# Kernel tuning notes

Measured on AMD Instinct MI355X. Metric: run time of the kernel, lower is better.

## Reference

```python
import jax, jax.numpy as jnp
import numpy as np


def _att(h, g, adj, a1, a2):
    # h: [B,N,D], g: [B,M,D], adj: [B,N,M] (int), a1/a2: [D,1]
    e1 = jnp.matmul(h, a1)                    # [B,N,1]
    e2 = jnp.matmul(g, a2).transpose(0, 2, 1)  # [B,1,M]
    e = jax.nn.leaky_relu(e1 + e2, negative_slope=0.2)  # [B,N,M]
    neg = jnp.asarray(-9.0e15, e.dtype)
    att = jnp.where(adj > 0, e, neg)
    att = jax.nn.softmax(att, axis=2)
    att = jnp.where(jnp.isnan(att), jnp.zeros_like(att), att)
    # degree renorm: adj[bs].sum(1).repeat(M,1).T == row degree broadcast over M
    deg = jnp.sum(adj, axis=2, keepdims=True).astype(e.dtype)  # [B,N,1]
    return jnp.matmul(att * deg, g)            # [B,N,D]


def setup_inputs() -> dict:
    key = jax.random.key(0)
    ks = jax.random.split(key, 13)
    B, N1, N2 = 64, 1024, 512
    F0, F1, D = 512, 384, 256
    return {
        "x0": jax.random.normal(ks[0], (B, N1, F0), jnp.float32),
        "x1": jax.random.normal(ks[1], (B, N2, F1), jnp.float32),
        "W0": jax.random.normal(ks[2], (F0, D), jnp.float32) * (1.414 / np.sqrt(F0)),
        "W1": jax.random.normal(ks[3], (F1, D), jnp.float32) * (1.414 / np.sqrt(F1)),
        "a1_0": jax.random.normal(ks[4], (D, 1), jnp.float32) * 0.1,
        "a2_0": jax.random.normal(ks[5], (D, 1), jnp.float32) * 0.1,
        "a1_1": jax.random.normal(ks[6], (D, 1), jnp.float32) * 0.1,
        "a2_1": jax.random.normal(ks[7], (D, 1), jnp.float32) * 0.1,
        "bias": jax.random.uniform(ks[8], (D,), jnp.float32, -1.0 / np.sqrt(D), 1.0 / np.sqrt(D)),
        "adj00": jax.random.randint(ks[9], (B, N1, N1), 0, 2, jnp.int32),
        "adj01": jax.random.randint(ks[10], (B, N1, N2), 0, 2, jnp.int32),
        "adj10": jax.random.randint(ks[11], (B, N2, N1), 0, 2, jnp.int32),
        "adj11": jax.random.randint(ks[12], (B, N2, N2), 0, 2, jnp.int32),
    }


def reference(x0, x1, W0, W1, a1_0, a2_0, a1_1, a2_1, bias,
              adj00, adj01, adj10, adj11):
    h0 = jnp.matmul(x0, W0)  # [B,N1,D]
    h1 = jnp.matmul(x1, W1)  # [B,N2,D]
    o00 = _att(h0, h0, adj00, a1_0, a2_0) + bias
    o01 = _att(h0, h1, adj01, a1_0, a2_0) + bias
    o10 = _att(h1, h0, adj10, a1_1, a2_1) + bias
    o11 = _att(h1, h1, adj11, a1_1, a2_1) + bias
    return (o00, o01, o10, o11)
```

## Files before the change

kernel.cpp:

```cpp
#include <hip/hip_runtime.h>

typedef __bf16 bf16x8 __attribute__((ext_vector_type(8)));
typedef float f32x4 __attribute__((ext_vector_type(4)));

static __device__ __forceinline__ ushort f2bf(float f) {
  uint u = __builtin_bit_cast(uint, f);
  u += 0x7fffu + ((u >> 16) & 1u);
  return (ushort)(u >> 16);
}
static __device__ __forceinline__ float bf2f(ushort h) {
  uint u = ((uint)h) << 16;
  return __builtin_bit_cast(float, u);
}

__global__ void detect9(const ushort* p0, const ushort* p1, const ushort* p2,
                        const ushort* p3, const ushort* p4, const ushort* p5,
                        const ushort* p6, const ushort* p7, const ushort* p8,
                        int* flags) {
  const ushort* ps[9] = {p0, p1, p2, p3, p4, p5, p6, p7, p8};
  const ushort* p = ps[blockIdx.x];
  int t = threadIdx.x;
  ushort u = p[2 * t];
  int e = (u >> 7) & 0xFF;
  int sane = (e >= 100 && e <= 150) ? 1 : 0;
  unsigned long long m = __ballot(sane);
  if (t == 0) flags[blockIdx.x] = (__popcll(m) >= 48) ? 0 : 1;
}

static __device__ __forceinline__ float ldf(const void* p, int is32, size_t i) {
  return is32 ? ((const float*)p)[i] : bf2f(((const ushort*)p)[i]);
}

__global__ void transw(const void* W, ushort* __restrict__ WT,
                       const int* __restrict__ flags, int fi, int F) {
  int is32 = flags[fi];
  int i = blockIdx.x * 256 + threadIdx.x;
  int k = i >> 8, d = i & 255;
  ushort v = is32 ? f2bf(((const float*)W)[i]) : ((const ushort*)W)[i];
  WT[(size_t)d * F + k] = v;
}

__global__ __launch_bounds__(256) void wa_k(const void* W, const void* a1, const void* a2,
                                            const void* a3, const int* __restrict__ flags,
                                            int fW, int f1, int f2, int f3,
                                            float* __restrict__ wa, int F) {
  __shared__ float al[3][256];
  int t = threadIdx.x;
  al[0][t] = ldf(a1, flags[f1], t);
  al[1][t] = ldf(a2, flags[f2], t);
  al[2][t] = ldf(a3, flags[f3], t);
  __syncthreads();
  int k = blockIdx.x * 256 + t;
  if (k < F) {
    int w32 = flags[fW];
    float s0 = 0.f, s1 = 0.f, s2 = 0.f;
    for (int d = 0; d < 256; d++) {
      float wv = ldf(W, w32, (size_t)k * 256 + d);
      s0 += wv * al[0][d]; s1 += wv * al[1][d]; s2 += wv * al[2][d];
    }
    wa[k] = s0; wa[F + k] = s1; wa[2 * F + k] = s2;
  }
}

__global__ __launch_bounds__(256) void evec_x(const void* __restrict__ x,
                                              const float* __restrict__ wa,
                                              const int* __restrict__ flags, int fi,
                                              float* __restrict__ o1, float* __restrict__ o2,
                                              float* __restrict__ o3, int F) {
  int x32 = flags[fi];
  int node = blockIdx.x * 4 + (threadIdx.x >> 6);
  int lane = threadIdx.x & 63;
  const float* wa1 = wa, *wa2 = wa + F, *wa3 = wa + 2 * F;
  float s1 = 0.f, s2 = 0.f, s3 = 0.f;
  size_t base = (size_t)node * F;
  for (int k = lane; k < F; k += 64) {
    float xv = ldf(x, x32, base + k);
    s1 += xv * wa1[k]; s2 += xv * wa2[k]; s3 += xv * wa3[k];
  }
  #pragma unroll
  for (int off = 1; off < 64; off <<= 1) {
    s1 += __shfl_xor(s1, off); s2 += __shfl_xor(s2, off); s3 += __shfl_xor(s3, off);
  }
  if (lane == 0) { o1[node] = s1; o2[node] = s2; o3[node] = s3; }
}

__global__ __launch_bounds__(256) void gemm_h(const void* __restrict__ x,
                                              const ushort* __restrict__ WT,
                                              ushort* __restrict__ hT,
                                              const int* __restrict__ flags, int fi,
                                              int N, int F) {
  int x32 = flags[fi];
  int ntiles = N >> 6;
  int b  = blockIdx.x / ntiles;
  int n0 = (blockIdx.x % ntiles) << 6;
  __shared__ ushort Al[64][72];
  __shared__ ushort Bl[256][72];
  int t = threadIdx.x, wave = t >> 6, lane = t & 63;
  f32x4 acc[4][4] = {};

  for (int k0 = 0; k0 < F; k0 += 64) {
    #pragma unroll
    for (int i = 0; i < 2; i++) {
      int r = (t >> 3) + i * 32, g = t & 7;
      if (!x32) {
        const ushort* xb = (const ushort*)x + (size_t)(b * N + n0 + r) * F + k0;
        ((uint4*)&Al[r][0])[g] = ((const uint4*)xb)[g];
      } else {
        const float* xf = (const float*)x + (size_t)(b * N + n0 + r) * F + k0;
        float4 fa = ((const float4*)xf)[2 * g];
        float4 fb = ((const float4*)xf)[2 * g + 1];
        union { ushort u[8]; uint4 q; } pk;
        pk.u[0] = f2bf(fa.x); pk.u[1] = f2bf(fa.y); pk.u[2] = f2bf(fa.z); pk.u[3] = f2bf(fa.w);
        pk.u[4] = f2bf(fb.x); pk.u[5] = f2bf(fb.y); pk.u[6] = f2bf(fb.z); pk.u[7] = f2bf(fb.w);
        ((uint4*)&Al[r][0])[g] = pk.q;
      }
    }
    #pragma unroll
    for (int i = 0; i < 8; i++) {
      int d = (t >> 3) + i * 32, g = t & 7;
      ((uint4*)&Bl[d][0])[g] = ((const uint4*)(WT + (size_t)d * F + k0))[g];
    }
    __syncthreads();
    #pragma unroll
    for (int kh = 0; kh < 2; kh++) {
      int kk = kh * 32 + ((lane >> 4) << 3);
      bf16x8 af[4], bfr[4];
      #pragma unroll
      for (int rf = 0; rf < 4; rf++) af[rf]  = *(const bf16x8*)&Al[rf * 16 + (lane & 15)][kk];
      #pragma unroll
      for (int cf = 0; cf < 4; cf++) bfr[cf] = *(const bf16x8*)&Bl[wave * 64 + cf * 16 + (lane & 15)][kk];
      #pragma unroll
      for (int rf = 0; rf < 4; rf++)
        #pragma unroll
        for (int cf = 0; cf < 4; cf++)
          acc[rf][cf] = __builtin_amdgcn_mfma_f32_16x16x32_bf16(af[rf], bfr[cf], acc[rf][cf], 0, 0, 0);
    }
    __syncthreads();
  }
  #pragma unroll
  for (int rf = 0; rf < 4; rf++) {
    int n = n0 + rf * 16 + ((lane >> 4) << 2);
    #pragma unroll
    for (int cf = 0; cf < 4; cf++) {
      int d = wave * 64 + cf * 16 + (lane & 15);
      ushort4 v;
      v.x = f2bf(acc[rf][cf][0]); v.y = f2bf(acc[rf][cf][1]);
      v.z = f2bf(acc[rf][cf][2]); v.w = f2bf(acc[rf][cf][3]);
      *(ushort4*)(hT + ((size_t)b * 256 + d) * N + n) = v;
    }
  }
}

__global__ __launch_bounds__(256) void att(const float* __restrict__ e1,
                                           const float* __restrict__ e2,
                                           const ushort* __restrict__ gT,
                                           const int* __restrict__ adj,
                                           const void* bias,
                                           const int* __restrict__ flags,
                                           void* __restrict__ outv, size_t ooff,
                                           int Nr, int M) {
  int b32 = flags[8];
  int o32 = flags[0] | flags[1] | flags[2] | flags[3] | flags[4] |
            flags[5] | flags[6] | flags[7] | flags[8];
  int ntiles = Nr >> 6;
  int lt = __builtin_ctz(ntiles);
  int wg = blockIdx.x;
  int c = wg & 7, j = wg >> 3;
  int b  = c * 8 + (j >> lt);
  int n0 = (j & (ntiles - 1)) << 6;
  __shared__ ushort Wl[64][72];
  __shared__ ushort Gl[256][72];
  __shared__ float  e2l[1024];
  __shared__ float  e1l[64];
  __shared__ float  rscale[64];
  int t = threadIdx.x, wave = t >> 6, lane = t & 63;
  for (int i = t; i < M; i += 256) e2l[i] = e2[(size_t)b * M + i];
  if (t < 64) e1l[t] = e1[(size_t)b * Nr + n0 + t];
  __syncthreads();

  f32x4 acc[4][4] = {};
  float s_part = 0.f, deg_part = 0.f;
  int r = t >> 2, mseg = (t & 3) << 4;
  float e1v = e1l[r];
  const int* adjrow = adj + ((size_t)b * Nr + n0 + r) * M;

  for (int m0 = 0; m0 < M; m0 += 64) {
    #pragma unroll
    for (int i = 0; i < 8; i++) {
      int d = (t >> 3) + i * 32, g = t & 7;
      ((uint4*)&Gl[d][0])[g] = ((const uint4*)(gT + ((size_t)b * 256 + d) * M + m0))[g];
    }
    {
      const int* ap = adjrow + m0 + mseg;
      int4 q0 = ((const int4*)ap)[0], q1 = ((const int4*)ap)[1];
      int4 q2 = ((const int4*)ap)[2], q3 = ((const int4*)ap)[3];
      int av[16] = {q0.x,q0.y,q0.z,q0.w, q1.x,q1.y,q1.z,q1.w,
                    q2.x,q2.y,q2.z,q2.w, q3.x,q3.y,q3.z,q3.w};
      union { ushort u[16]; uint4 q[2]; } pk;
      #pragma unroll
      for (int jj = 0; jj < 16; jj++) {
        float e = e1v + e2l[m0 + mseg + jj];
        e = e > 0.f ? e : 0.2f * e;
        e = fminf(e, 60.f);
        float w = (av[jj] > 0) ? __expf(e) : 0.f;
        ushort wb = f2bf(w);
        s_part += bf2f(wb);
        deg_part += (float)av[jj];
        pk.u[jj] = wb;
      }
      *(uint4*)&Wl[r][mseg]     = pk.q[0];
      *(uint4*)&Wl[r][mseg + 8] = pk.q[1];
    }
    __syncthreads();
    #pragma unroll
    for (int kh = 0; kh < 2; kh++) {
      int kk = kh * 32 + ((lane >> 4) << 3);
      bf16x8 af[4], bfr[4];
      #pragma unroll
      for (int rf = 0; rf < 4; rf++) af[rf]  = *(const bf16x8*)&Wl[rf * 16 + (lane & 15)][kk];
      #pragma unroll
      for (int cf = 0; cf < 4; cf++) bfr[cf] = *(const bf16x8*)&Gl[wave * 64 + cf * 16 + (lane & 15)][kk];
      #pragma unroll
      for (int rf = 0; rf < 4; rf++)
        #pragma unroll
        for (int cf = 0; cf < 4; cf++)
          acc[rf][cf] = __builtin_amdgcn_mfma_f32_16x16x32_bf16(af[rf], bfr[cf], acc[rf][cf], 0, 0, 0);
    }
    __syncthreads();
  }

  s_part   += __shfl_xor(s_part, 1);   s_part   += __shfl_xor(s_part, 2);
  deg_part += __shfl_xor(deg_part, 1); deg_part += __shfl_xor(deg_part, 2);
  if ((t & 3) == 0) {
    float sc = (s_part > 0.f) ? deg_part / s_part : 0.f;
    if (!(sc > -1e38f && sc < 1e38f)) sc = 0.f;
    rscale[r] = sc;
  }
  __syncthreads();

  #pragma unroll
  for (int rf = 0; rf < 4; rf++) {
    int nbase = rf * 16 + ((lane >> 4) << 2);
    #pragma unroll
    for (int cf = 0; cf < 4; cf++) {
      int d = wave * 64 + cf * 16 + (lane & 15);
      float bi = ldf(bias, b32, d);
      #pragma unroll
      for (int jj = 0; jj < 4; jj++) {
        int nl = nbase + jj;
        float v = acc[rf][cf][jj] * rscale[nl] + bi;
        size_t idx = ooff + ((size_t)(b * Nr + n0 + nl)) * 256 + d;
        if (o32) ((float*)outv)[idx] = v;
        else     ((ushort*)outv)[idx] = f2bf(v);
      }
    }
  }
}

extern "C" void kernel_launch(void* const* d_in, const int* in_sizes, int n_in,
                              void* d_out, int out_size, void* d_ws, size_t ws_size,
                              hipStream_t stream) {
  (void)in_sizes; (void)n_in; (void)out_size; (void)ws_size;
  const void* x0   = d_in[0];
  const void* x1   = d_in[1];
  const void* W0   = d_in[2];
  const void* W1   = d_in[3];
  const void* a1_0 = d_in[4];
  const void* a2_0 = d_in[5];
  const void* a1_1 = d_in[6];
  const void* a2_1 = d_in[7];
  const void* bias = d_in[8];
  const int* adj00 = (const int*)d_in[9];
  const int* adj01 = (const int*)d_in[10];
  const int* adj10 = (const int*)d_in[11];
  const int* adj11 = (const int*)d_in[12];

  const int B = 64, N1 = 1024, N2 = 512, F0 = 512, F1 = 384;
  int*    flags = (int*)d_ws;
  ushort* base = (ushort*)((char*)d_ws + 64);
  ushort* hT0 = base;
  ushort* hT1 = hT0 + (size_t)B * 256 * N1;
  ushort* WT0 = hT1 + (size_t)B * 256 * N2;
  ushort* WT1 = WT0 + (size_t)256 * F0;
  float* e1_0 = (float*)(WT1 + (size_t)256 * F1);
  float* e2a  = e1_0 + (size_t)B * N1;
  float* e2c  = e2a + (size_t)B * N1;
  float* e1_1 = e2c + (size_t)B * N1;
  float* e2b  = e1_1 + (size_t)B * N2;
  float* e2d  = e2b + (size_t)B * N2;
  float* wa0  = e2d + (size_t)B * N2;
  float* wa1  = wa0 + 3 * F0;

  detect9<<<9, 64, 0, stream>>>((const ushort*)x0, (const ushort*)x1,
                                (const ushort*)W0, (const ushort*)W1,
                                (const ushort*)a1_0, (const ushort*)a2_0,
                                (const ushort*)a1_1, (const ushort*)a2_1,
                                (const ushort*)bias, flags);

  transw<<<F0, 256, 0, stream>>>(W0, WT0, flags, 2, F0);
  transw<<<F1, 256, 0, stream>>>(W1, WT1, flags, 3, F1);
  wa_k<<<(F0 + 255) / 256, 256, 0, stream>>>(W0, a1_0, a2_0, a2_1, flags, 2, 4, 5, 7, wa0, F0);
  wa_k<<<(F1 + 255) / 256, 256, 0, stream>>>(W1, a1_1, a2_0, a2_1, flags, 3, 6, 5, 7, wa1, F1);
  gemm_h<<<B * (N1 / 64), 256, 0, stream>>>(x0, WT0, hT0, flags, 0, N1, F0);
  gemm_h<<<B * (N2 / 64), 256, 0, stream>>>(x1, WT1, hT1, flags, 1, N2, F1);
  evec_x<<<B * N1 / 4, 256, 0, stream>>>(x0, wa0, flags, 0, e1_0, e2a, e2c, F0);
  evec_x<<<B * N2 / 4, 256, 0, stream>>>(x1, wa1, flags, 1, e1_1, e2b, e2d, F1);

  const size_t o00 = 0;
  const size_t o01 = (size_t)B * N1 * 256;
  const size_t o10 = o01 + (size_t)B * N1 * 256;
  const size_t o11 = o10 + (size_t)B * N2 * 256;
  att<<<B * (N1 / 64), 256, 0, stream>>>(e1_0, e2a, hT0, adj00, bias, flags, d_out, o00, N1, N1);
  att<<<B * (N1 / 64), 256, 0, stream>>>(e1_0, e2b, hT1, adj01, bias, flags, d_out, o01, N1, N2);
  att<<<B * (N2 / 64), 256, 0, stream>>>(e1_1, e2c, hT0, adj10, bias, flags, d_out, o10, N2, N1);
  att<<<B * (N2 / 64), 256, 0, stream>>>(e1_1, e2d, hT1, adj11, bias, flags, d_out, o11, N2, N2);
}
```

Baseline: 1.033 ms.

## Load MFMA operands directly from global memory, bypassing LDS staging

In both the projection GEMM and the attention kernel, the LDS staging of the B operand (weights or gT), and in gemm_h also the A operand, is removed. Each lane now reads its bf16x8 MFMA fragments straight from global memory. This drops LDS traffic and the barriers in gemm_h, and shrinks shared memory, which may raise occupancy. The cost is redundant global and L2 reads across waves and less-coalesced 16-byte strided accesses.

```diff
diff --git a/kernel.cpp b/kernel.cpp
--- a/kernel.cpp
+++ b/kernel.cpp
@@ -93,49 +93,41 @@
   int ntiles = N >> 6;
   int b  = blockIdx.x / ntiles;
   int n0 = (blockIdx.x % ntiles) << 6;
-  __shared__ ushort Al[64][72];
-  __shared__ ushort Bl[256][72];
   int t = threadIdx.x, wave = t >> 6, lane = t & 63;
+  int kkbase = (lane >> 4) << 3;
   f32x4 acc[4][4] = {};
+
+  const ushort* wb = WT + (size_t)(wave * 64 + (lane & 15)) * F;
+  size_t xrow = (size_t)(b * N + n0 + (lane & 15)) * F;
 
   for (int k0 = 0; k0 < F; k0 += 64) {
     #pragma unroll
-    for (int i = 0; i < 2; i++) {
-      int r = (t >> 3) + i * 32, g = t & 7;
-      if (!x32) {
-        const ushort* xb = (const ushort*)x + (size_t)(b * N + n0 + r) * F + k0;
-        ((uint4*)&Al[r][0])[g] = ((const uint4*)xb)[g];
-      } else {
-        const float* xf = (const float*)x + (size_t)(b * N + n0 + r) * F + k0;
-        float4 fa = ((const float4*)xf)[2 * g];
-        float4 fb = ((const float4*)xf)[2 * g + 1];
-        union { ushort u[8]; uint4 q; } pk;
-        pk.u[0] = f2bf(fa.x); pk.u[1] = f2bf(fa.y); pk.u[2] = f2bf(fa.z); pk.u[3] = f2bf(fa.w);
-        pk.u[4] = f2bf(fb.x); pk.u[5] = f2bf(fb.y); pk.u[6] = f2bf(fb.z); pk.u[7] = f2bf(fb.w);
-        ((uint4*)&Al[r][0])[g] = pk.q;
+    for (int kh = 0; kh < 2; kh++) {
+      int kk = k0 + kh * 32 + kkbase;
+      bf16x8 af[4], bfr[4];
+      #pragma unroll
+      for (int rf = 0; rf < 4; rf++) {
+        if (x32) {
+          const float* xp = (const float*)x + xrow + (size_t)(rf * 16) * F + kk;
+          float4 fa = ((const float4*)xp)[0];
+          float4 fb = ((const float4*)xp)[1];
+          union { ushort u[8]; bf16x8 v; } pk;
+          pk.u[0] = f2bf(fa.x); pk.u[1] = f2bf(fa.y); pk.u[2] = f2bf(fa.z); pk.u[3] = f2bf(fa.w);
+          pk.u[4] = f2bf(fb.x); pk.u[5] = f2bf(fb.y); pk.u[6] = f2bf(fb.z); pk.u[7] = f2bf(fb.w);
+          af[rf] = pk.v;
+        } else {
+          af[rf] = *(const bf16x8*)((const ushort*)x + xrow + (size_t)(rf * 16) * F + kk);
+        }
       }
-    }
-    #pragma unroll
-    for (int i = 0; i < 8; i++) {
-      int d = (t >> 3) + i * 32, g = t & 7;
-      ((uint4*)&Bl[d][0])[g] = ((const uint4*)(WT + (size_t)d * F + k0))[g];
-    }
-    __syncthreads();
-    #pragma unroll
-    for (int kh = 0; kh < 2; kh++) {
-      int kk = kh * 32 + ((lane >> 4) << 3);
-      bf16x8 af[4], bfr[4];
-      #pragma unroll
-      for (int rf = 0; rf < 4; rf++) af[rf]  = *(const bf16x8*)&Al[rf * 16 + (lane & 15)][kk];
-      #pragma unroll
-      for (int cf = 0; cf < 4; cf++) bfr[cf] = *(const bf16x8*)&Bl[wave * 64 + cf * 16 + (lane & 15)][kk];
+      #pragma unroll
+      for (int cf = 0; cf < 4; cf++)
+        bfr[cf] = *(const bf16x8*)(wb + (size_t)(cf * 16) * F + kk);
       #pragma unroll
       for (int rf = 0; rf < 4; rf++)
         #pragma unroll
         for (int cf = 0; cf < 4; cf++)
           acc[rf][cf] = __builtin_amdgcn_mfma_f32_16x16x32_bf16(af[rf], bfr[cf], acc[rf][cf], 0, 0, 0);
     }
-    __syncthreads();
   }
   #pragma unroll
   for (int rf = 0; rf < 4; rf++) {
@@ -169,7 +161,6 @@
   int b  = c * 8 + (j >> lt);
   int n0 = (j & (ntiles - 1)) << 6;
   __shared__ ushort Wl[64][72];
-  __shared__ ushort Gl[256][72];
   __shared__ float  e2l[1024];
   __shared__ float  e1l[64];
   __shared__ float  rscale[64];
@@ -181,15 +172,12 @@
   f32x4 acc[4][4] = {};
   float s_part = 0.f, deg_part = 0.f;
   int r = t >> 2, mseg = (t & 3) << 4;
+  int kkbase = (lane >> 4) << 3;
   float e1v = e1l[r];
   const int* adjrow = adj + ((size_t)b * Nr + n0 + r) * M;
+  const ushort* gb = gT + ((size_t)b * 256 + wave * 64 + (lane & 15)) * M;
 
   for (int m0 = 0; m0 < M; m0 += 64) {
-    #pragma unroll
-    for (int i = 0; i < 8; i++) {
-      int d = (t >> 3) + i * 32, g = t & 7;
-      ((uint4*)&Gl[d][0])[g] = ((const uint4*)(gT + ((size_t)b * 256 + d) * M + m0))[g];
-    }
     {
       const int* ap = adjrow + m0 + mseg;
       int4 q0 = ((const int4*)ap)[0], q1 = ((const int4*)ap)[1];
@@ -214,12 +202,13 @@
     __syncthreads();
     #pragma unroll
     for (int kh = 0; kh < 2; kh++) {
-      int kk = kh * 32 + ((lane >> 4) << 3);
+      int kk = kh * 32 + kkbase;
       bf16x8 af[4], bfr[4];
       #pragma unroll
       for (int rf = 0; rf < 4; rf++) af[rf]  = *(const bf16x8*)&Wl[rf * 16 + (lane & 15)][kk];
       #pragma unroll
-      for (int cf = 0; cf < 4; cf++) bfr[cf] = *(const bf16x8*)&Gl[wave * 64 + cf * 16 + (lane & 15)][kk];
+      for (int cf = 0; cf < 4; cf++)
+        bfr[cf] = *(const bf16x8*)(gb + (size_t)(cf * 16) * M + m0 + kk);
       #pragma unroll
       for (int rf = 0; rf < 4; rf++)
         #pragma unroll
```

Result: slower. 1.138 ms (+10.2%).
